# Performance work log

Hardware: AMD Instinct MI355X
Metric: run time of the kernel (lower is better)

## Reference

```python
import jax, jax.numpy as jnp
import numpy as np

NUM_HEADS, NUM_KV_HEADS, HEAD_DIM, HIDDEN = 8, 1, 256, 2048
B, S = 1, 4096

def setup_inputs() -> dict:
    key = jax.random.key(0)
    ks = jax.random.split(key, 6)
    sd = 1.0 / np.sqrt(HIDDEN)
    x = jax.random.normal(ks[0], (B, S, HIDDEN), dtype=jnp.float32)
    wq = jax.random.normal(ks[1], (HIDDEN, NUM_HEADS, HEAD_DIM), dtype=jnp.float32) * sd
    bq = jnp.zeros((NUM_HEADS, HEAD_DIM), dtype=jnp.float32)
    wkv = jax.random.normal(ks[2], (HIDDEN, NUM_KV_HEADS, HEAD_DIM), dtype=jnp.float32) * sd
    bkv = jnp.zeros((NUM_KV_HEADS, HEAD_DIM), dtype=jnp.float32)
    wo = jax.random.normal(ks[3], (NUM_HEADS, HEAD_DIM, HIDDEN), dtype=jnp.float32) / np.sqrt(NUM_HEADS * HEAD_DIM)
    bo = jnp.zeros((HIDDEN,), dtype=jnp.float32)
    # causal mask, broadcastable to [b, h, q, k]
    mask = jnp.tril(jnp.ones((S, S), dtype=bool))[None, None, :, :]
    return {"x": x, "wq": wq, "bq": bq, "wkv": wkv, "bkv": bkv, "wo": wo, "bo": bo, "mask": mask}

def reference(x, wq, bq, wkv, bkv, wo, bo, mask):
    # q: [b,s,h,d]; kv: [b,s,kvh,d] -- used as BOTH k and v (as in source)
    q = jnp.einsum('bsh,hnd->bsnd', x, wq) + bq
    kv = jnp.einsum('bsh,hnd->bsnd', x, wkv) + bkv
    q = jnp.transpose(q, (0, 2, 1, 3))   # [b,h,s,d]
    k = jnp.transpose(kv, (0, 2, 1, 3))  # [b,kvh,s,d]
    v = k
    rep = NUM_HEADS // NUM_KV_HEADS
    k = jnp.repeat(k, rep, axis=1)
    v = jnp.repeat(v, rep, axis=1)
    scale = 1.0 / jnp.sqrt(jnp.float32(HEAD_DIM))
    attn = jnp.einsum('bhqd,bhkd->bhqk', q, k) * scale
    attn = jnp.where(mask, attn, -1e9)
    attn = jax.nn.softmax(attn, axis=-1)
    out = jnp.einsum('bhqk,bhkd->bhqd', attn, v)
    out = jnp.transpose(out, (0, 2, 1, 3))  # [b,s,h,d]
    return jnp.einsum('bsnd,ndh->bsh', out, wo) + bo
```

## Files before the change

kernel.cpp:

```cpp
#include <hip/hip_runtime.h>
#include <hip/hip_bf16.h>
#include <stdint.h>

#define HIDDEN 2048
#define SEQ 4096
#define NH 8
#define HD 256

typedef float f32x4 __attribute__((ext_vector_type(4)));
typedef short s16x8 __attribute__((ext_vector_type(8)));
typedef float f32x4v __attribute__((ext_vector_type(4)));

#define QSCALE 0.09016844005556021f

__device__ inline uint16_t f2bf(float f) {
  union { float f; uint32_t u; } v;
  v.f = f;
  uint32_t r = (v.u + 0x7fffu + ((v.u >> 16) & 1u)) >> 16;
  return (uint16_t)r;
}

__device__ inline void gll16(const uint16_t* src, uint16_t* lds) {
  __builtin_amdgcn_global_load_lds(
      (const __attribute__((address_space(1))) unsigned int*)src,
      (__attribute__((address_space(3))) unsigned int*)lds, 16, 0, 0);
}

__global__ __launch_bounds__(256) void cast_kernel(const float* __restrict__ in,
                                                   uint16_t* __restrict__ out, int n4) {
  int i = blockIdx.x * 256 + threadIdx.x;
  if (i >= n4) return;
  f32x4v v = ((const f32x4v*)in)[i];
  union { uint16_t u[4]; uint64_t l; } o;
  o.u[0] = f2bf(v.x); o.u[1] = f2bf(v.y); o.u[2] = f2bf(v.z); o.u[3] = f2bf(v.w);
  ((uint64_t*)out)[i] = o.l;
}

__global__ __launch_bounds__(256) void transpose_cast_kernel(const float* __restrict__ in,
                                                             uint16_t* __restrict__ out,
                                                             int R, int C) {
  __shared__ uint16_t tile[64][65];
  int t = threadIdx.x;
  int ctiles = C >> 6;
  int c0 = (blockIdx.x % ctiles) << 6;
  int r0 = (blockIdx.x / ctiles) << 6;
#pragma unroll
  for (int p = 0; p < 16; ++p) {
    int r = p * 4 + (t >> 6), c = t & 63;
    tile[c][r] = f2bf(in[(size_t)(r0 + r) * C + c0 + c]);
  }
  __syncthreads();
#pragma unroll
  for (int p = 0; p < 16; ++p) {
    int r = p * 4 + (t >> 6), c = t & 63;
    out[(size_t)(c0 + r) * R + r0 + c] = tile[r][c];
  }
}

__device__ inline void gemm_tile_core(const uint16_t* __restrict__ A,
                                      const uint16_t* __restrict__ BT, int K, int m0,
                                      uint16_t* Alds, uint16_t* Blds, f32x4 acc[4][4]) {
  const int t = threadIdx.x, lane = t & 63, wid = t >> 6;
  const int l15 = lane & 15, l4 = lane >> 4;
  const int wm = wid >> 1, wn = wid & 1;
#pragma unroll
  for (int i = 0; i < 4; ++i)
#pragma unroll
    for (int j = 0; j < 4; ++j) acc[i][j] = f32x4{0.f, 0.f, 0.f, 0.f};

  auto stage = [&](int kt, int b) {
#pragma unroll
    for (int i = 0; i < 2; ++i) {
      int j = i * 256 + t;
      gll16(A + (size_t)(m0 + (j >> 2)) * K + kt + (j & 3) * 8,
            Alds + b * 4096 + (i * 256 + wid * 64) * 8);
    }
#pragma unroll
    for (int i = 0; i < 2; ++i) {
      int j = i * 256 + t;
      gll16(BT + (size_t)(j >> 2) * K + kt + (j & 3) * 8,
            Blds + b * 4096 + (i * 256 + wid * 64) * 8);
    }
  };

  stage(0, 0);
  int b = 0;
  for (int kt = 0; kt < K; kt += 32, b ^= 1) {
    __syncthreads();
    if (kt + 32 < K) stage(kt + 32, b ^ 1);
    s16x8 av[4], bv[4];
#pragma unroll
    for (int mi = 0; mi < 4; ++mi)
      av[mi] = *(const s16x8*)(Alds + b * 4096 + (wm * 64 + mi * 16 + l15) * 32 + l4 * 8);
#pragma unroll
    for (int nj = 0; nj < 4; ++nj)
      bv[nj] = *(const s16x8*)(Blds + b * 4096 + (wn * 64 + nj * 16 + l15) * 32 + l4 * 8);
#pragma unroll
    for (int mi = 0; mi < 4; ++mi)
#pragma unroll
      for (int nj = 0; nj < 4; ++nj)
        acc[mi][nj] = __builtin_amdgcn_mfma_f32_16x16x32_bf16(av[mi], bv[nj],
                                                              acc[mi][nj], 0, 0, 0);
  }
}

__global__ __launch_bounds__(256) void gemm_qkv_kernel(
    const uint16_t* __restrict__ xb, const uint16_t* __restrict__ wqT,
    const uint16_t* __restrict__ wkvT, const float* __restrict__ bq,
    const float* __restrict__ bkv, uint16_t* __restrict__ Qws,
    uint16_t* __restrict__ Kws, uint16_t* __restrict__ VTws) {
  __shared__ uint16_t Alds[8192], Blds[8192];
  int b0 = blockIdx.x;
  int bid = (b0 & 7) * 72 + (b0 >> 3);
  int bn = bid % 18, bm = bid / 18;
  int m0 = bm * 128;
  const uint16_t* BT = (bn < 16) ? (wqT + (size_t)bn * 128 * HIDDEN)
                                 : (wkvT + (size_t)(bn - 16) * 128 * HIDDEN);
  f32x4 acc[4][4];
  gemm_tile_core(xb, BT, HIDDEN, m0, Alds, Blds, acc);
  const int lane = threadIdx.x & 63, wid = threadIdx.x >> 6;
  const int l15 = lane & 15, l4 = lane >> 4;
  const int wm = wid >> 1, wn = wid & 1;
#pragma unroll
  for (int mi = 0; mi < 4; ++mi) {
#pragma unroll
    for (int nj = 0; nj < 4; ++nj) {
      int nloc = bn * 128 + wn * 64 + nj * 16 + l15;
#pragma unroll
      for (int r = 0; r < 4; ++r) {
        int m = m0 + wm * 64 + mi * 16 + 4 * l4 + r;
        float v = acc[mi][nj][r];
        if (bn < 16) {
          v = (v + bq[nloc]) * QSCALE;
          uint16_t b = f2bf(v);
          int head = nloc >> 8, d = nloc & 255;
          Qws[((size_t)head * SEQ + m) * HD + d] = b;
        } else {
          int d = nloc - 2048;
          v += bkv[d];
          uint16_t b = f2bf(v);
          Kws[(size_t)m * HD + d] = b;
          VTws[(size_t)d * SEQ + m] = b;
        }
      }
    }
  }
}

__global__ __launch_bounds__(256) void attn_kernel(const uint16_t* __restrict__ Qws,
                                                   const uint16_t* __restrict__ Kws,
                                                   const uint16_t* __restrict__ VTws,
                                                   uint16_t* __restrict__ Ows) {
  __shared__ unsigned char smem[140288];
  const int t = threadIdx.x, lane = t & 63, wid = t >> 6;
  const int l15 = lane & 15, l4 = lane >> 4;
  const int h = blockIdx.x & 7, p = blockIdx.x >> 3;
  uint16_t* Pw = (uint16_t*)(smem + 131072 + wid * 2304);

  auto stageKV = [&](int kb, int buf) {
    uint16_t* Klds = (uint16_t*)(smem + buf * 32768);
#pragma unroll
    for (int i = 0; i < 8; ++i) {
      int j = i * 256 + t;
      int r = j >> 5, cp = j & 31;
      int c = (cp & ~7) | ((cp ^ r) & 7);
      gll16(Kws + (size_t)(kb * 64 + r) * HD + c * 8, Klds + (i * 256 + wid * 64) * 8);
    }
    uint16_t* VTlds = (uint16_t*)(smem + 65536 + buf * 32768);
#pragma unroll
    for (int i = 0; i < 8; ++i) {
      int j = i * 256 + t;
      int d = j >> 3, cp = j & 7;
      int c = (cp ^ d) & 7;
      gll16(VTws + (size_t)d * SEQ + kb * 64 + c * 8, VTlds + (i * 256 + wid * 64) * 8);
    }
  };

  for (int half = 0; half < 2; ++half) {
    const int qb = half ? p : 63 - p;
    const int qrow = qb * 64 + wid * 16 + l15;

    s16x8 qf[8];
    const uint16_t* qbase = Qws + ((size_t)h * SEQ + qrow) * HD;
#pragma unroll
    for (int kk = 0; kk < 8; ++kk) qf[kk] = *(const s16x8*)(qbase + kk * 32 + l4 * 8);

    float mrun = -1e30f, lrun = 0.f;
    f32x4 oacc[16];
#pragma unroll
    for (int i = 0; i < 16; ++i) oacc[i] = f32x4{0.f, 0.f, 0.f, 0.f};

    const int nt = qb + 1;
    __syncthreads();
    stageKV(0, 0);

    for (int kb = 0; kb < nt; ++kb) {
      const int buf = kb & 1;
      __syncthreads();
      if (kb + 1 < nt) stageKV(kb + 1, buf ^ 1);
      uint16_t* Klds = (uint16_t*)(smem + buf * 32768);
      uint16_t* VTlds = (uint16_t*)(smem + 65536 + buf * 32768);

      f32x4 sacc[4];
#pragma unroll
      for (int i = 0; i < 4; ++i) sacc[i] = f32x4{0.f, 0.f, 0.f, 0.f};
#pragma unroll
      for (int kvt = 0; kvt < 4; ++kvt) {
#pragma unroll
        for (int kk = 0; kk < 8; ++kk) {
          int r = kvt * 16 + l15;
          int c = kk * 4 + l4;
          int cs = (c & ~7) | ((c ^ r) & 7);
          s16x8 kf = *(const s16x8*)(Klds + r * 256 + cs * 8);
          sacc[kvt] = __builtin_amdgcn_mfma_f32_16x16x32_bf16(kf, qf[kk], sacc[kvt], 0, 0, 0);
        }
      }

      float pv[16];
      float vmax = -1e30f;
      const bool diag = (kb == qb);
#pragma unroll
      for (int kvt = 0; kvt < 4; ++kvt) {
#pragma unroll
        for (int r = 0; r < 4; ++r) {
          float s = sacc[kvt][r];
          if (diag) {
            int kv = kb * 64 + kvt * 16 + 4 * l4 + r;
            if (kv > qrow) s = -1e30f;
          }
          pv[kvt * 4 + r] = s;
          vmax = fmaxf(vmax, s);
        }
      }
      vmax = fmaxf(vmax, __shfl_xor(vmax, 16));
      vmax = fmaxf(vmax, __shfl_xor(vmax, 32));

      if (!__all(vmax - mrun <= 8.0f)) {
        float mnew = fmaxf(mrun, vmax);
        float alpha = exp2f(mrun - mnew);
        float a4[4];
#pragma unroll
        for (int r = 0; r < 4; ++r) a4[r] = __shfl(alpha, 4 * l4 + r);
#pragma unroll
        for (int dt = 0; dt < 16; ++dt) {
#pragma unroll
          for (int r = 0; r < 4; ++r) oacc[dt][r] *= a4[r];
        }
        lrun *= alpha;
        mrun = mnew;
      }
      float rsum = 0.f;
#pragma unroll
      for (int i = 0; i < 16; ++i) {
        float pe = exp2f(pv[i] - mrun);
        pv[i] = pe;
        rsum += pe;
      }
      rsum += __shfl_xor(rsum, 16);
      rsum += __shfl_xor(rsum, 32);
      lrun += rsum;

#pragma unroll
      for (int kvt = 0; kvt < 4; ++kvt) {
        uint64_t pk = (uint64_t)f2bf(pv[kvt * 4 + 0]) |
                      ((uint64_t)f2bf(pv[kvt * 4 + 1]) << 16) |
                      ((uint64_t)f2bf(pv[kvt * 4 + 2]) << 32) |
                      ((uint64_t)f2bf(pv[kvt * 4 + 3]) << 48);
        *(uint64_t*)(Pw + l15 * 72 + kvt * 16 + l4 * 4) = pk;
      }
#pragma unroll
      for (int kk = 0; kk < 2; ++kk) {
        s16x8 pa = *(const s16x8*)(Pw + l15 * 72 + kk * 32 + l4 * 8);
#pragma unroll
        for (int dt = 0; dt < 16; ++dt) {
          int d = dt * 16 + l15;
          int c = (kk * 4 + l4) ^ (d & 7);
          s16x8 vf = *(const s16x8*)(VTlds + d * 64 + c * 8);
          oacc[dt] = __builtin_amdgcn_mfma_f32_16x16x32_bf16(pa, vf, oacc[dt], 0, 0, 0);
        }
      }
    }

    float linv = 1.0f / lrun;
    float li4[4];
#pragma unroll
    for (int r = 0; r < 4; ++r) li4[r] = __shfl(linv, 4 * l4 + r);
#pragma unroll
    for (int dt = 0; dt < 16; ++dt) {
#pragma unroll
      for (int r = 0; r < 4; ++r) {
        int s = qb * 64 + wid * 16 + 4 * l4 + r;
        int col = h * HD + dt * 16 + l15;
        Ows[(size_t)s * HIDDEN + col] = f2bf(oacc[dt][r] * li4[r]);
      }
    }
  }
}

__global__ __launch_bounds__(256) void gemm_out_kernel(const uint16_t* __restrict__ Ows,
                                                       const uint16_t* __restrict__ woT,
                                                       const float* __restrict__ bo,
                                                       float* __restrict__ Y) {
  __shared__ uint16_t Alds[8192], Blds[8192];
  int b0 = blockIdx.x;
  int bid = (b0 & 7) * 64 + (b0 >> 3);
  int bn = bid % 16, bm = bid / 16;
  int m0 = bm * 128;
  f32x4 acc[4][4];
  gemm_tile_core(Ows, woT + (size_t)bn * 128 * HIDDEN, HIDDEN, m0, Alds, Blds, acc);
  const int lane = threadIdx.x & 63, wid = threadIdx.x >> 6;
  const int l15 = lane & 15, l4 = lane >> 4;
  const int wm = wid >> 1, wn = wid & 1;
#pragma unroll
  for (int mi = 0; mi < 4; ++mi) {
#pragma unroll
    for (int nj = 0; nj < 4; ++nj) {
      int n = bn * 128 + wn * 64 + nj * 16 + l15;
      float bias = bo[n];
#pragma unroll
      for (int r = 0; r < 4; ++r) {
        int m = m0 + wm * 64 + mi * 16 + 4 * l4 + r;
        Y[(size_t)m * HIDDEN + n] = acc[mi][nj][r] + bias;
      }
    }
  }
}

extern "C" void kernel_launch(void* const* d_in, const int* in_sizes, int n_in,
                              void* d_out, int out_size, void* d_ws, size_t ws_size,
                              hipStream_t stream) {
  const float* x = (const float*)d_in[0];
  const float* wq = (const float*)d_in[1];
  const float* bq = (const float*)d_in[2];
  const float* wkv = (const float*)d_in[3];
  const float* bkv = (const float*)d_in[4];
  const float* wo = (const float*)d_in[5];
  const float* bo = (const float*)d_in[6];
  float* Y = (float*)d_out;

  uint8_t* ws = (uint8_t*)d_ws;
  uint16_t* xb   = (uint16_t*)(ws + 0);
  uint16_t* wqT  = (uint16_t*)(ws + 16777216);
  uint16_t* wkvT = (uint16_t*)(ws + 25165824);
  uint16_t* woT  = (uint16_t*)(ws + 26214400);
  uint16_t* Qws  = (uint16_t*)(ws + 34603008);
  uint16_t* Kws  = (uint16_t*)(ws + 51380224);
  uint16_t* VTws = (uint16_t*)(ws + 53477376);
  uint16_t* Ows  = (uint16_t*)(ws + 55574528);

  cast_kernel<<<8192, 256, 0, stream>>>(x, xb, (SEQ * HIDDEN) / 4);
  transpose_cast_kernel<<<1024, 256, 0, stream>>>(wq, wqT, HIDDEN, 2048);
  transpose_cast_kernel<<<128, 256, 0, stream>>>(wkv, wkvT, HIDDEN, 256);
  transpose_cast_kernel<<<1024, 256, 0, stream>>>(wo, woT, 2048, HIDDEN);
  gemm_qkv_kernel<<<32 * 18, 256, 0, stream>>>(xb, wqT, wkvT, bq, bkv, Qws, Kws, VTws);
  attn_kernel<<<256, 256, 0, stream>>>(Qws, Kws, VTws, Ows);
  gemm_out_kernel<<<32 * 16, 256, 0, stream>>>(Ows, woT, bo, Y);
}
```

Baseline: 442.5 us.

## Split attention into one q-block per workgroup, single-buffer LDS, precompute offsets

The attention kernel no longer processes two paired query blocks per workgroup. It launches 512 workgroups, one q-block each, with the longest blocks scheduled first. LDS drops from double-buffered (~140KB) to single-buffered (~75KB) so two workgroups can share a CU, and swizzled LDS offsets are precomputed per lane. P is packed to bf16 with the hardware v_cvt_pk_bf16_f32 instruction. The trade-off is that global loads for the next KV tile no longer overlap compute within a workgroup, so overlap must come from the extra resident workgroups, and tail balance now depends on the hardware scheduler.

```diff
diff --git a/kernel.cpp b/kernel.cpp
--- a/kernel.cpp
+++ b/kernel.cpp
@@ -10,6 +10,7 @@
 typedef float f32x4 __attribute__((ext_vector_type(4)));
 typedef short s16x8 __attribute__((ext_vector_type(8)));
 typedef float f32x4v __attribute__((ext_vector_type(4)));
+typedef unsigned int u32x2 __attribute__((ext_vector_type(2)));
 
 #define QSCALE 0.09016844005556021f
 
@@ -18,6 +19,12 @@
   v.f = f;
   uint32_t r = (v.u + 0x7fffu + ((v.u >> 16) & 1u)) >> 16;
   return (uint16_t)r;
+}
+
+__device__ inline uint32_t cvtpk(float a, float b) {
+  uint32_t r;
+  asm("v_cvt_pk_bf16_f32 %0, %1, %2" : "=v"(r) : "v"(a), "v"(b));
+  return r;
 }
 
 __device__ inline void gll16(const uint16_t* src, uint16_t* lds) {
@@ -151,14 +158,32 @@
                                                    const uint16_t* __restrict__ Kws,
                                                    const uint16_t* __restrict__ VTws,
                                                    uint16_t* __restrict__ Ows) {
-  __shared__ unsigned char smem[140288];
+  __shared__ unsigned char smem[74752];
+  uint16_t* Klds = (uint16_t*)smem;
+  uint16_t* VTlds = (uint16_t*)(smem + 32768);
   const int t = threadIdx.x, lane = t & 63, wid = t >> 6;
   const int l15 = lane & 15, l4 = lane >> 4;
-  const int h = blockIdx.x & 7, p = blockIdx.x >> 3;
-  uint16_t* Pw = (uint16_t*)(smem + 131072 + wid * 2304);
-
-  auto stageKV = [&](int kb, int buf) {
-    uint16_t* Klds = (uint16_t*)(smem + buf * 32768);
+  const int b = blockIdx.x;
+  const int h = b & 7, p = (b >> 3) & 31;
+  const int qb = (b < 256) ? (63 - p) : p;
+  const int qrow = qb * 64 + wid * 16 + l15;
+  uint16_t* Pw = (uint16_t*)(smem + 65536 + wid * 2304);
+
+  int koff[8];
+#pragma unroll
+  for (int kk = 0; kk < 8; ++kk) {
+    int c = kk * 4 + l4;
+    int cs = (c & ~7) | ((c ^ l15) & 7);
+    koff[kk] = l15 * 512 + cs * 16;
+  }
+  int voff[2];
+#pragma unroll
+  for (int kk = 0; kk < 2; ++kk) {
+    int c = (kk * 4 + l4) ^ (l15 & 7);
+    voff[kk] = l15 * 128 + c * 16;
+  }
+
+  auto stageKV = [&](int kb) {
 #pragma unroll
     for (int i = 0; i < 8; ++i) {
       int j = i * 256 + t;
@@ -166,7 +191,6 @@
       int c = (cp & ~7) | ((cp ^ r) & 7);
       gll16(Kws + (size_t)(kb * 64 + r) * HD + c * 8, Klds + (i * 256 + wid * 64) * 8);
     }
-    uint16_t* VTlds = (uint16_t*)(smem + 65536 + buf * 32768);
 #pragma unroll
     for (int i = 0; i < 8; ++i) {
       int j = i * 256 + t;
@@ -176,123 +200,112 @@
     }
   };
 
-  for (int half = 0; half < 2; ++half) {
-    const int qb = half ? p : 63 - p;
-    const int qrow = qb * 64 + wid * 16 + l15;
-
-    s16x8 qf[8];
-    const uint16_t* qbase = Qws + ((size_t)h * SEQ + qrow) * HD;
-#pragma unroll
-    for (int kk = 0; kk < 8; ++kk) qf[kk] = *(const s16x8*)(qbase + kk * 32 + l4 * 8);
-
-    float mrun = -1e30f, lrun = 0.f;
-    f32x4 oacc[16];
-#pragma unroll
-    for (int i = 0; i < 16; ++i) oacc[i] = f32x4{0.f, 0.f, 0.f, 0.f};
-
-    const int nt = qb + 1;
+  s16x8 qf[8];
+  const uint16_t* qbase = Qws + ((size_t)h * SEQ + qrow) * HD;
+#pragma unroll
+  for (int kk = 0; kk < 8; ++kk) qf[kk] = *(const s16x8*)(qbase + kk * 32 + l4 * 8);
+
+  float mrun = -1e30f, lrun = 0.f;
+  f32x4 oacc[16];
+#pragma unroll
+  for (int i = 0; i < 16; ++i) oacc[i] = f32x4{0.f, 0.f, 0.f, 0.f};
+
+  const int nt = qb + 1;
+  stageKV(0);
+
+  for (int kb = 0; kb < nt; ++kb) {
     __syncthreads();
-    stageKV(0, 0);
-
-    for (int kb = 0; kb < nt; ++kb) {
-      const int buf = kb & 1;
+
+    f32x4 sacc[4];
+#pragma unroll
+    for (int i = 0; i < 4; ++i) sacc[i] = f32x4{0.f, 0.f, 0.f, 0.f};
+#pragma unroll
+    for (int kvt = 0; kvt < 4; ++kvt) {
+#pragma unroll
+      for (int kk = 0; kk < 8; ++kk) {
+        s16x8 kf = *(const s16x8*)((const unsigned char*)Klds + kvt * 8192 + koff[kk]);
+        sacc[kvt] = __builtin_amdgcn_mfma_f32_16x16x32_bf16(kf, qf[kk], sacc[kvt], 0, 0, 0);
+      }
+    }
+
+    float pv[16];
+    float vmax = -1e30f;
+    const bool diag = (kb == qb);
+#pragma unroll
+    for (int kvt = 0; kvt < 4; ++kvt) {
+#pragma unroll
+      for (int r = 0; r < 4; ++r) {
+        float s = sacc[kvt][r];
+        if (diag) {
+          int kv = kb * 64 + kvt * 16 + 4 * l4 + r;
+          if (kv > qrow) s = -1e30f;
+        }
+        pv[kvt * 4 + r] = s;
+        vmax = fmaxf(vmax, s);
+      }
+    }
+    vmax = fmaxf(vmax, __shfl_xor(vmax, 16));
+    vmax = fmaxf(vmax, __shfl_xor(vmax, 32));
+
+    if (!__all(vmax - mrun <= 8.0f)) {
+      float mnew = fmaxf(mrun, vmax);
+      float alpha = exp2f(mrun - mnew);
+      float a4[4];
+#pragma unroll
+      for (int r = 0; r < 4; ++r) a4[r] = __shfl(alpha, 4 * l4 + r);
+#pragma unroll
+      for (int dt = 0; dt < 16; ++dt) {
+#pragma unroll
+        for (int r = 0; r < 4; ++r) oacc[dt][r] *= a4[r];
+      }
+      lrun *= alpha;
+      mrun = mnew;
+    }
+    float rsum = 0.f;
+#pragma unroll
+    for (int i = 0; i < 16; ++i) {
+      float pe = exp2f(pv[i] - mrun);
+      pv[i] = pe;
+      rsum += pe;
+    }
+    rsum += __shfl_xor(rsum, 16);
+    rsum += __shfl_xor(rsum, 32);
+    lrun += rsum;
+
+#pragma unroll
+    for (int kvt = 0; kvt < 4; ++kvt) {
+      u32x2 w;
+      w.x = cvtpk(pv[kvt * 4 + 0], pv[kvt * 4 + 1]);
+      w.y = cvtpk(pv[kvt * 4 + 2], pv[kvt * 4 + 3]);
+      *(u32x2*)(Pw + l15 * 72 + kvt * 16 + l4 * 4) = w;
+    }
+#pragma unroll
+    for (int kk = 0; kk < 2; ++kk) {
+      s16x8 pa = *(const s16x8*)(Pw + l15 * 72 + kk * 32 + l4 * 8);
+#pragma unroll
+      for (int dt = 0; dt < 16; ++dt) {
+        s16x8 vf = *(const s16x8*)((const unsigned char*)VTlds + dt * 2048 + voff[kk]);
+        oacc[dt] = __builtin_amdgcn_mfma_f32_16x16x32_bf16(pa, vf, oacc[dt], 0, 0, 0);
+      }
+    }
+
+    if (kb + 1 < nt) {
       __syncthreads();
-      if (kb + 1 < nt) stageKV(kb + 1, buf ^ 1);
-      uint16_t* Klds = (uint16_t*)(smem + buf * 32768);
-      uint16_t* VTlds = (uint16_t*)(smem + 65536 + buf * 32768);
-
-      f32x4 sacc[4];
-#pragma unroll
-      for (int i = 0; i < 4; ++i) sacc[i] = f32x4{0.f, 0.f, 0.f, 0.f};
-#pragma unroll
-      for (int kvt = 0; kvt < 4; ++kvt) {
-#pragma unroll
-        for (int kk = 0; kk < 8; ++kk) {
-          int r = kvt * 16 + l15;
-          int c = kk * 4 + l4;
-          int cs = (c & ~7) | ((c ^ r) & 7);
-          s16x8 kf = *(const s16x8*)(Klds + r * 256 + cs * 8);
-          sacc[kvt] = __builtin_amdgcn_mfma_f32_16x16x32_bf16(kf, qf[kk], sacc[kvt], 0, 0, 0);
-        }
-      }
-
-      float pv[16];
-      float vmax = -1e30f;
-      const bool diag = (kb == qb);
-#pragma unroll
-      for (int kvt = 0; kvt < 4; ++kvt) {
-#pragma unroll
-        for (int r = 0; r < 4; ++r) {
-          float s = sacc[kvt][r];
-          if (diag) {
-            int kv = kb * 64 + kvt * 16 + 4 * l4 + r;
-            if (kv > qrow) s = -1e30f;
-          }
-          pv[kvt * 4 + r] = s;
-          vmax = fmaxf(vmax, s);
-        }
-      }
-      vmax = fmaxf(vmax, __shfl_xor(vmax, 16));
-      vmax = fmaxf(vmax, __shfl_xor(vmax, 32));
-
-      if (!__all(vmax - mrun <= 8.0f)) {
-        float mnew = fmaxf(mrun, vmax);
-        float alpha = exp2f(mrun - mnew);
-        float a4[4];
-#pragma unroll
-        for (int r = 0; r < 4; ++r) a4[r] = __shfl(alpha, 4 * l4 + r);
-#pragma unroll
-        for (int dt = 0; dt < 16; ++dt) {
-#pragma unroll
-          for (int r = 0; r < 4; ++r) oacc[dt][r] *= a4[r];
-        }
-        lrun *= alpha;
-        mrun = mnew;
-      }
-      float rsum = 0.f;
-#pragma unroll
-      for (int i = 0; i < 16; ++i) {
-        float pe = exp2f(pv[i] - mrun);
-        pv[i] = pe;
-        rsum += pe;
-      }
-      rsum += __shfl_xor(rsum, 16);
-      rsum += __shfl_xor(rsum, 32);
-      lrun += rsum;
-
-#pragma unroll
-      for (int kvt = 0; kvt < 4; ++kvt) {
-        uint64_t pk = (uint64_t)f2bf(pv[kvt * 4 + 0]) |
-                      ((uint64_t)f2bf(pv[kvt * 4 + 1]) << 16) |
-                      ((uint64_t)f2bf(pv[kvt * 4 + 2]) << 32) |
-                      ((uint64_t)f2bf(pv[kvt * 4 + 3]) << 48);
-        *(uint64_t*)(Pw + l15 * 72 + kvt * 16 + l4 * 4) = pk;
-      }
-#pragma unroll
-      for (int kk = 0; kk < 2; ++kk) {
-        s16x8 pa = *(const s16x8*)(Pw + l15 * 72 + kk * 32 + l4 * 8);
-#pragma unroll
-        for (int dt = 0; dt < 16; ++dt) {
-          int d = dt * 16 + l15;
-          int c = (kk * 4 + l4) ^ (d & 7);
-          s16x8 vf = *(const s16x8*)(VTlds + d * 64 + c * 8);
-          oacc[dt] = __builtin_amdgcn_mfma_f32_16x16x32_bf16(pa, vf, oacc[dt], 0, 0, 0);
-        }
-      }
-    }
-
-    float linv = 1.0f / lrun;
-    float li4[4];
-#pragma unroll
-    for (int r = 0; r < 4; ++r) li4[r] = __shfl(linv, 4 * l4 + r);
-#pragma unroll
-    for (int dt = 0; dt < 16; ++dt) {
-#pragma unroll
-      for (int r = 0; r < 4; ++r) {
-        int s = qb * 64 + wid * 16 + 4 * l4 + r;
-        int col = h * HD + dt * 16 + l15;
-        Ows[(size_t)s * HIDDEN + col] = f2bf(oacc[dt][r] * li4[r]);
-      }
+      stageKV(kb + 1);
+    }
+  }
+
+  float linv = 1.0f / lrun;
+  float li4[4];
+#pragma unroll
+  for (int r = 0; r < 4; ++r) li4[r] = __shfl(linv, 4 * l4 + r);
+#pragma unroll
+  for (int dt = 0; dt < 16; ++dt) {
+#pragma unroll
+    for (int r = 0; r < 4; ++r) {
+      int s = qb * 64 + wid * 16 + 4 * l4 + r;
+      int col = h * HD + dt * 16 + l15;
+      Ows[(size_t)s * HIDDEN + col] = f2bf(oacc[dt][r] * li4[r]);
     }
   }
 }
@@ -353,6 +366,6 @@
   transpose_cast_kernel<<<128, 256, 0, stream>>>(wkv, wkvT, HIDDEN, 256);
   transpose_cast_kernel<<<1024, 256, 0, stream>>>(wo, woT, 2048, HIDDEN);
   gemm_qkv_kernel<<<32 * 18, 256, 0, stream>>>(xb, wqT, wkvT, bq, bkv, Qws, Kws, VTws);
-  attn_kernel<<<256, 256, 0, stream>>>(Qws, Kws, VTws, Ows);
+  attn_kernel<<<512, 256, 0, stream>>>(Qws, Kws, VTws, Ows);
   gemm_out_kernel<<<32 * 16, 256, 0, stream>>>(Ows, woT, bo, Y);
 }
```

Result: slower. 486.2 us (+9.9%).
